# Kernel tuning notes

Hardware: AMD Instinct MI355X
Metric: run time of the kernel (lower is better)

The kernel has to match this reference:

```python
import jax, jax.numpy as jnp
import numpy as np

LAYERS, HIDDEN, FFN, HEADS = 2, 128, 256, 4
IMG_H, IMG_W = 32, 64
SEQ = IMG_H * IMG_W
HEAD = HIDDEN // HEADS          # 32, per-head qk dim
HEAD_V = 2 * HEAD               # double_v_dim=True
VDIM = HEADS * HEAD_V           # 256
B = 2
SCALE_BASE = 512.0
EPS = 1e-5


def _xpos_tables(seq, d):
    # XPOS: rotary angles + per-position exponential scale
    half = d // 2
    scale_vec = (jnp.arange(0, d, 2, dtype=jnp.float32) + 0.4 * d) / (1.4 * d)  # (d/2,)
    power = jnp.arange(seq, dtype=jnp.float32) / SCALE_BASE
    scale = scale_vec[None, :] ** power[:, None]                                 # (S, d/2)
    inv_freq = 1.0 / (10000.0 ** (jnp.arange(half, dtype=jnp.float32) / half))
    ang = jnp.arange(seq, dtype=jnp.float32)[:, None] * inv_freq[None, :]        # (S, d/2)
    return jnp.sin(ang), jnp.cos(ang), scale


def _apply_xpos(x, sin, cos, scale):
    # duplicate-interleave sin/cos*scale to width d, rotate-every-two
    s = jnp.repeat(sin * scale, 2, axis=-1)   # (S, d)
    c = jnp.repeat(cos * scale, 2, axis=-1)
    x1, x2 = x[..., ::2], x[..., 1::2]
    rot = jnp.stack([-x2, x1], axis=-1).reshape(x.shape)
    return x * c + rot * s


def _ln(x, g, b):
    mu = x.mean(-1, keepdims=True)
    var = ((x - mu) ** 2).mean(-1, keepdims=True)
    return (x - mu) * jax.lax.rsqrt(var + EPS) * g + b


def _gn(y, g, b):
    # GroupNorm(HEADS groups) over VDIM channels, applied per token
    bsz, s, v = y.shape
    yg = y.reshape(bsz, s, HEADS, HEAD_V)
    mu = yg.mean(-1, keepdims=True)
    var = ((yg - mu) ** 2).mean(-1, keepdims=True)
    yn = ((yg - mu) * jax.lax.rsqrt(var + EPS)).reshape(bsz, s, v)
    return yn * g + b


def _decay(seq):
    # D[h, n, m] = gamma_h^(n-m) for n >= m else 0
    gammas = 1.0 - jnp.exp(jnp.linspace(jnp.log(1.0 / 32.0), jnp.log(1.0 / 512.0), HEADS))
    n = jnp.arange(seq, dtype=jnp.float32)
    diff = n[:, None] - n[None, :]
    return (gammas[:, None, None] ** jnp.maximum(diff, 0.0)) * (diff >= 0.0)


def _forward(x, ln1_g, ln1_b, ln2_g, ln2_b, WQ, WK, WV, WG, WO, gn_g, gn_b, w1, b1, w2, b2):
    sin, cos, scale = _xpos_tables(SEQ, HEAD)
    D = _decay(SEQ)  # (H, S, S)
    for i in range(LAYERS):
        h = _ln(x, ln1_g[i], ln1_b[i])
        Q = _apply_xpos(jnp.einsum('bsd,hde->bhse', h, WQ[i]), sin, cos, scale)
        K = _apply_xpos(jnp.einsum('bsd,hde->bhse', h, WK[i]), sin, cos, 1.0 / scale)
        V = jnp.einsum('bsd,hdv->bhsv', h, WV[i])
        att = jnp.einsum('bhse,bhte->bhst', Q, K) * D[None]      # decay retention
        Y = jnp.einsum('bhst,bhtv->bhsv', att, V)
        Y = jnp.moveaxis(Y, 1, 2).reshape(x.shape[0], SEQ, VDIM)  # concat heads
        Y = _gn(Y, gn_g[i], gn_b[i])
        G = h @ WG[i]
        ret = (G * jax.nn.sigmoid(G) * Y) @ WO[i]                 # swish gate + out proj
        y = ret + x
        h2 = _ln(y, ln2_g[i], ln2_b[i])
        x = jax.nn.gelu(h2 @ w1[i] + b1[i], approximate=False) @ w2[i] + b2[i] + y
    return x.reshape(x.shape[0], IMG_H, IMG_W, x.shape[-1])


def setup_inputs() -> dict:
    key = jax.random.key(0)
    ks = jax.random.split(key, 8)
    def rn(k, shape, sc):
        return jax.random.normal(k, shape, dtype=jnp.float32) * sc
    s = 1.0 / np.sqrt(HIDDEN)
    return {
        'x': rn(ks[0], (B, SEQ, HIDDEN), 1.0),
        'ln1_g': jnp.ones((LAYERS, HIDDEN), jnp.float32),
        'ln1_b': jnp.zeros((LAYERS, HIDDEN), jnp.float32),
        'ln2_g': jnp.ones((LAYERS, HIDDEN), jnp.float32),
        'ln2_b': jnp.zeros((LAYERS, HIDDEN), jnp.float32),
        'WQ': rn(ks[1], (LAYERS, HEADS, HIDDEN, HEAD), s),
        'WK': rn(ks[2], (LAYERS, HEADS, HIDDEN, HEAD), s),
        'WV': rn(ks[3], (LAYERS, HEADS, HIDDEN, HEAD_V), s),
        'WG': rn(ks[4], (LAYERS, HIDDEN, VDIM), s),
        'WO': rn(ks[5], (LAYERS, VDIM, HIDDEN), 1.0 / np.sqrt(VDIM)),
        'gn_g': jnp.ones((LAYERS, VDIM), jnp.float32),
        'gn_b': jnp.zeros((LAYERS, VDIM), jnp.float32),
        'w1': rn(ks[6], (LAYERS, HIDDEN, FFN), s),
        'b1': jnp.zeros((LAYERS, FFN), jnp.float32),
        'w2': rn(ks[7], (LAYERS, FFN, HIDDEN), 1.0 / np.sqrt(FFN)),
        'b2': jnp.zeros((LAYERS, HIDDEN), jnp.float32),
    }


def reference(x, ln1_g, ln1_b, ln2_g, ln2_b, WQ, WK, WV, WG, WO, gn_g, gn_b, w1, b1, w2, b2):
    return _forward(x, ln1_g, ln1_b, ln2_g, ln2_b, WQ, WK, WV, WG, WO, gn_g, gn_b, w1, b1, w2, b2)
```

## Files before the change

### kernel.cpp

```cpp
#include <hip/hip_runtime.h>
#include <math.h>

#define NLAYERS 2
#define HID 128
#define FFND 256
#define NH 4
#define SEQL 2048
#define HD 32
#define HDV 64
#define VD 256
#define NBATCH 2
#define MROWS (NBATCH*SEQL)
#define NCAT 768
#define NCHUNK 32

__global__ __launch_bounds__(256) void setup_kernel(
    const float* __restrict__ WQ, const float* __restrict__ WK,
    const float* __restrict__ WV, const float* __restrict__ WG,
    float* __restrict__ Wcat, float* __restrict__ tabs)
{
  int bid = blockIdx.x;
  if (bid < 768) {
    int idx = bid * 256 + threadIdx.x;
    int l = idx / (HID * NCAT);
    int r = idx - l * (HID * NCAT);
    int k = r / NCAT;
    int n = r - k * NCAT;
    float v;
    if (n < 128)      { int h = n >> 5, e = n & 31;            v = WQ[(((l*NH+h)*HID)+k)*HD  + e]; }
    else if (n < 256) { int m = n-128; int h = m>>5, e = m&31; v = WK[(((l*NH+h)*HID)+k)*HD  + e]; }
    else if (n < 512) { int m = n-256; int h = m>>6, e = m&63; v = WV[(((l*NH+h)*HID)+k)*HDV + e]; }
    else              { v = WG[(l*HID + k)*VD + (n-512)]; }
    Wcat[idx] = v;
  } else {
    int idx = (bid - 768) * 256 + threadIdx.x;
    int s = idx >> 4, i = idx & 15;
    float inv_freq = powf(10000.f, -(float)i * (1.f/16.f));
    float ang = (float)s * inv_freq;
    float sv  = ((float)(2*i) + 0.4f*32.f) / (1.4f*32.f);
    float sc  = powf(sv, (float)s * (1.f/512.f));
    float sn = sinf(ang), cs = cosf(ang);
    tabs[idx]          = sn * sc;
    tabs[32768 + idx]  = cs * sc;
    tabs[65536 + idx]  = sn / sc;
    tabs[98304 + idx]  = cs / sc;
  }
}

template<int CN, bool XPOS, bool BIAS, bool GELU>
__global__ __launch_bounds__(256) void gemm_ln(
    const float* __restrict__ A, const float* __restrict__ Bw,
    const float* __restrict__ lng, const float* __restrict__ lnb,
    const float* __restrict__ bias, const float* __restrict__ tabs,
    float* __restrict__ C, int N)
{
  constexpr int TN = 16 * CN;
  constexpr int BK = (CN == 8) ? 32 : 64;
  __shared__ float As[128][68];
  __shared__ float Bs[BK][TN + 4];

  int tid = threadIdx.x;
  int tx = tid & 15, ty = tid >> 4;
  int rb = blockIdx.x * 64, nb = blockIdx.y * TN;

  {
    int row = tid >> 2, q = tid & 3;
    const float* ar = A + (size_t)(rb + row) * HID + 32 * q;
    float4 av[8];
    #pragma unroll
    for (int it = 0; it < 8; it++) av[it] = *(const float4*)(ar + 4*it);
    float s = 0.f;
    #pragma unroll
    for (int it = 0; it < 8; it++) s += av[it].x + av[it].y + av[it].z + av[it].w;
    s += __shfl_xor(s, 1); s += __shfl_xor(s, 2);
    float mu = s * (1.f/128.f);
    float qs = 0.f;
    #pragma unroll
    for (int it = 0; it < 8; it++) {
      float d;
      d = av[it].x - mu; qs += d*d;  d = av[it].y - mu; qs += d*d;
      d = av[it].z - mu; qs += d*d;  d = av[it].w - mu; qs += d*d;
    }
    qs += __shfl_xor(qs, 1); qs += __shfl_xor(qs, 2);
    float rs = rsqrtf(qs * (1.f/128.f) + 1e-5f);
    int rsw = row ^ (16 * q);
    #pragma unroll
    for (int it = 0; it < 8; it++) {
      int k0 = 32*q + 4*it;
      float4 g4 = *(const float4*)(lng + k0);
      float4 b4 = *(const float4*)(lnb + k0);
      As[k0+0][rsw] = (av[it].x-mu)*rs*g4.x + b4.x;
      As[k0+1][rsw] = (av[it].y-mu)*rs*g4.y + b4.y;
      As[k0+2][rsw] = (av[it].z-mu)*rs*g4.z + b4.z;
      As[k0+3][rsw] = (av[it].w-mu)*rs*g4.w + b4.w;
    }
  }

  float acc[4][CN];
  #pragma unroll
  for (int i=0;i<4;i++)
    #pragma unroll
    for (int j=0;j<CN;j++) acc[i][j] = 0.f;

  for (int ks = 0; ks < 128; ks += BK) {
    #pragma unroll
    for (int it = 0; it < 4; it++) {
      int idx = it*256 + tid;
      int kk = idx / (TN/4), nq = idx % (TN/4);
      *(float4*)(&Bs[kk][4*nq]) =
          *(const float4*)(Bw + (size_t)(ks+kk)*N + nb + 4*nq);
    }
    __syncthreads();
    #pragma unroll
    for (int kk = 0; kk < BK; kk++) {
      int k = ks + kk;
      float a[4];
      *(float4*)a = *(const float4*)&As[k][(4*ty) ^ (16*(k>>5))];
      float b[CN];
      #pragma unroll
      for (int j4 = 0; j4 < CN; j4 += 4)
        *(float4*)(b+j4) = *(const float4*)&Bs[kk][CN*tx + j4];
      #pragma unroll
      for (int i=0;i<4;i++)
        #pragma unroll
        for (int j=0;j<CN;j++)
          acc[i][j] = fmaf(a[i], b[j], acc[i][j]);
    }
    __syncthreads();
  }

  #pragma unroll
  for (int i=0;i<4;i++) {
    int row = rb + 4*ty + i;
    int cb = nb + CN*tx;
    float o[CN];
    #pragma unroll
    for (int j=0;j<CN;j++) {
      float v = acc[i][j];
      if (BIAS)  v += bias[cb + j];
      if (GELU)  v = 0.5f * v * (1.f + erff(v * 0.70710678118f));
      o[j] = v;
    }
    if (XPOS) {
      if (nb < 256) {
        bool isK = (nb >= 128);
        const float* sn_t = tabs + (isK ? 65536 : 0);
        const float* cs_t = tabs + (isK ? 98304 : 32768);
        int s = row & (SEQL - 1);
        #pragma unroll
        for (int p = 0; p < CN/2; p++) {
          int i0 = ((cb + 2*p) & 31) >> 1;
          float sn = sn_t[s*16 + i0], cs = cs_t[s*16 + i0];
          float x1 = o[2*p], x2 = o[2*p+1];
          o[2*p]   = x1*cs - x2*sn;
          o[2*p+1] = x2*cs + x1*sn;
        }
      }
    }
    #pragma unroll
    for (int j4 = 0; j4 < CN; j4 += 4)
      *(float4*)(C + (size_t)row*N + cb + j4) = *(float4*)(o + j4);
  }
}

template<bool BIAS>
__global__ __launch_bounds__(256) void gemm_nar(
    const float* __restrict__ A, const float* __restrict__ Bw,
    const float* __restrict__ bias, const float* __restrict__ Rsd,
    float* __restrict__ C, int N)
{
  __shared__ float As[64][68];
  __shared__ float Bs[64][36];
  int tid = threadIdx.x;
  int tx = tid & 15, ty = tid >> 4;
  int rb = blockIdx.x * 64, nb = blockIdx.y * 32;

  float acc[4][2];
  #pragma unroll
  for (int i=0;i<4;i++) { acc[i][0]=0.f; acc[i][1]=0.f; }

  for (int ks = 0; ks < 256; ks += 64) {
    #pragma unroll
    for (int it = 0; it < 4; it++) {
      int idx = it*256 + tid;
      int row = idx >> 4, kq = idx & 15;
      float4 a4 = *(const float4*)(A + (size_t)(rb+row)*256 + ks + 4*kq);
      int rsw = row ^ (4*(kq & 7));
      As[4*kq+0][rsw] = a4.x; As[4*kq+1][rsw] = a4.y;
      As[4*kq+2][rsw] = a4.z; As[4*kq+3][rsw] = a4.w;
    }
    #pragma unroll
    for (int it = 0; it < 2; it++) {
      int idx = it*256 + tid;
      int kk = idx >> 3, nq = idx & 7;
      *(float4*)(&Bs[kk][4*nq]) =
          *(const float4*)(Bw + (size_t)(ks+kk)*N + nb + 4*nq);
    }
    __syncthreads();
    #pragma unroll
    for (int kk = 0; kk < 64; kk++) {
      float a[4];
      *(float4*)a = *(const float4*)&As[kk][(4*ty) ^ (4*((kk>>2)&7))];
      float2 b2 = *(const float2*)&Bs[kk][2*tx];
      #pragma unroll
      for (int i=0;i<4;i++) {
        acc[i][0] = fmaf(a[i], b2.x, acc[i][0]);
        acc[i][1] = fmaf(a[i], b2.y, acc[i][1]);
      }
    }
    __syncthreads();
  }

  #pragma unroll
  for (int i=0;i<4;i++) {
    int row = rb + 4*ty + i;
    int cb = nb + 2*tx;
    float o[2];
    #pragma unroll
    for (int j=0;j<2;j++) {
      float v = acc[i][j];
      if (BIAS) v += bias[cb + j];
      v += Rsd[(size_t)row*N + cb + j];
      o[j] = v;
    }
    *(float2*)(C + (size_t)row*N + cb) = *(float2*)o;
  }
}

__global__ __launch_bounds__(512) void ret_kv_kernel(
    const float* __restrict__ QKVG, float* __restrict__ Asum)
{
  int bh = blockIdx.x >> 5;
  int c  = blockIdx.x & 31;
  int b = bh >> 2, h = bh & 3;
  float t0 = logf(1.f/32.f) + (float)h * (logf(1.f/512.f) - logf(1.f/32.f)) * (1.f/3.f);
  float gamma = 1.f - expf(t0);
  float lg = logf(gamma);

  __shared__ float Ks[64][36];
  __shared__ float Vs[64][68];
  __shared__ float wt[64];

  int tid = threadIdx.x;
  int c0 = c * 64;
  const float* base = QKVG + (size_t)(b * SEQL) * NCAT;

  {
    int row = tid >> 3, eq = tid & 7;
    *(float4*)&Ks[row][4*eq] =
        *(const float4*)(base + (size_t)(c0+row)*NCAT + 128 + h*32 + 4*eq);
  }
  #pragma unroll
  for (int it = 0; it < 2; it++) {
    int idx = it*512 + tid;
    int row = idx >> 4, vq = idx & 15;
    *(float4*)&Vs[row][4*vq] =
        *(const float4*)(base + (size_t)(c0+row)*NCAT + 256 + h*64 + 4*vq);
  }
  if (tid < 64) wt[tid] = __expf(lg * (float)(64 - tid));
  __syncthreads();

  int e = tid >> 4, v4 = (tid & 15) * 4;
  float a0[4] = {0,0,0,0};
  #pragma unroll 8
  for (int t = 0; t < 64; t++) {
    float kw = Ks[t][e] * wt[t];
    float4 v0 = *(const float4*)&Vs[t][v4];
    a0[0] = fmaf(kw, v0.x, a0[0]); a0[1] = fmaf(kw, v0.y, a0[1]);
    a0[2] = fmaf(kw, v0.z, a0[2]); a0[3] = fmaf(kw, v0.w, a0[3]);
  }
  *(float4*)(Asum + ((size_t)(bh*NCHUNK + c))*2048 + e*64 + v4) = *(float4*)a0;
}

__global__ __launch_bounds__(512) void ret_out_kernel(
    const float* __restrict__ QKVG, const float* __restrict__ Asum,
    const float* __restrict__ gn_g, const float* __restrict__ gn_b,
    float* __restrict__ Gated)
{
  int bh = blockIdx.x >> 5;
  int c  = blockIdx.x & 31;
  int b = bh >> 2, h = bh & 3;
  float t0 = logf(1.f/32.f) + (float)h * (logf(1.f/512.f) - logf(1.f/32.f)) * (1.f/3.f);
  float gamma = 1.f - expf(t0);
  float lg = logf(gamma);
  float g64 = __expf(lg * 64.f);

  __shared__ float Qs[64][36];
  __shared__ float Ks[64][36];
  __shared__ float Vs[64][68];
  __shared__ float Ss[64][68];
  __shared__ float Sc[32][68];

  int tid = threadIdx.x;
  int tx2 = tid & 31, ty2 = tid >> 5;
  int c0 = c * 64;
  const float* base = QKVG + (size_t)(b * SEQL) * NCAT;

  {
    int row = tid >> 3, eq = tid & 7;
    *(float4*)&Qs[row][4*eq] =
        *(const float4*)(base + (size_t)(c0+row)*NCAT + h*32 + 4*eq);
    int esw = (4*eq) ^ (4*((row >> 2) & 7));
    *(float4*)&Ks[row][esw] =
        *(const float4*)(base + (size_t)(c0+row)*NCAT + 128 + h*32 + 4*eq);
  }
  #pragma unroll
  for (int it = 0; it < 2; it++) {
    int idx = it*512 + tid;
    int row = idx >> 4, vq = idx & 15;
    *(float4*)&Vs[row][4*vq] =
        *(const float4*)(base + (size_t)(c0+row)*NCAT + 256 + h*64 + 4*vq);
  }

  {
    int e = tid >> 4, v4 = (tid & 15) * 4;
    float s0[4] = {0,0,0,0};
    float w = 1.f;
    const float* ab = Asum + ((size_t)bh*NCHUNK)*2048 + e*64 + v4;
    for (int cp = c-1; cp >= 0; --cp) {
      const float* ap = ab + (size_t)cp*2048;
      float4 x0 = *(const float4*)ap;
      s0[0] = fmaf(w, x0.x, s0[0]); s0[1] = fmaf(w, x0.y, s0[1]);
      s0[2] = fmaf(w, x0.z, s0[2]); s0[3] = fmaf(w, x0.w, s0[3]);
      w *= g64;
    }
    *(float4*)&Sc[e][v4] = *(float4*)s0;
  }
  __syncthreads();

  float sacc[4][2];
  #pragma unroll
  for (int i=0;i<4;i++) { sacc[i][0]=0.f; sacc[i][1]=0.f; }
  #pragma unroll
  for (int e = 0; e < 32; e += 4) {
    float qv[4][4], kv[2][4];
    #pragma unroll
    for (int i=0;i<4;i++)
      *(float4*)qv[i] = *(const float4*)&Qs[4*ty2+i][e];
    #pragma unroll
    for (int j=0;j<2;j++) {
      int kr = 2*tx2 + j;
      *(float4*)kv[j] = *(const float4*)&Ks[kr][e ^ (4*((kr>>2)&7))];
    }
    #pragma unroll
    for (int i=0;i<4;i++)
      #pragma unroll
      for (int j=0;j<2;j++)
        sacc[i][j] = fmaf(qv[i][0], kv[j][0],
                     fmaf(qv[i][1], kv[j][1],
                     fmaf(qv[i][2], kv[j][2],
                     fmaf(qv[i][3], kv[j][3], sacc[i][j]))));
  }
  #pragma unroll
  for (int i=0;i<4;i++) {
    int sl = 4*ty2 + i;
    float o2[2];
    #pragma unroll
    for (int j=0;j<2;j++) {
      int dr = sl - (2*tx2 + j);
      float w = (dr >= 0) ? __expf(lg * (float)dr) : 0.f;
      o2[j] = sacc[i][j] * w;
    }
    *(float2*)&Ss[sl][2*tx2] = *(float2*)o2;
  }

  float acc[4][2];
  #pragma unroll
  for (int i=0;i<4;i++) { acc[i][0]=0.f; acc[i][1]=0.f; }
  #pragma unroll
  for (int e = 0; e < 32; e += 4) {
    float qv[4][4], sv[4][2];
    #pragma unroll
    for (int i=0;i<4;i++)
      *(float4*)qv[i] = *(const float4*)&Qs[4*ty2+i][e];
    #pragma unroll
    for (int m=0;m<4;m++)
      *(float2*)sv[m] = *(const float2*)&Sc[e+m][2*tx2];
    #pragma unroll
    for (int i=0;i<4;i++)
      #pragma unroll
      for (int j=0;j<2;j++)
        acc[i][j] = fmaf(qv[i][0], sv[0][j],
                    fmaf(qv[i][1], sv[1][j],
                    fmaf(qv[i][2], sv[2][j],
                    fmaf(qv[i][3], sv[3][j], acc[i][j]))));
  }
  #pragma unroll
  for (int i=0;i<4;i++) {
    float gr = __expf(lg * (float)(4*ty2 + i));
    acc[i][0] *= gr; acc[i][1] *= gr;
  }
  __syncthreads();

  #pragma unroll
  for (int t = 0; t < 64; t += 4) {
    float sv[4][4], vv[4][2];
    #pragma unroll
    for (int i=0;i<4;i++)
      *(float4*)sv[i] = *(const float4*)&Ss[4*ty2+i][t];
    #pragma unroll
    for (int m=0;m<4;m++)
      *(float2*)vv[m] = *(const float2*)&Vs[t+m][2*tx2];
    #pragma unroll
    for (int i=0;i<4;i++)
      #pragma unroll
      for (int j=0;j<2;j++)
        acc[i][j] = fmaf(sv[i][0], vv[0][j],
                    fmaf(sv[i][1], vv[1][j],
                    fmaf(sv[i][2], vv[2][j],
                    fmaf(sv[i][3], vv[3][j], acc[i][j]))));
  }

  #pragma unroll
  for (int i=0;i<4;i++) {
    float s1 = acc[i][0] + acc[i][1];
    #pragma unroll
    for (int o = 16; o; o >>= 1) s1 += __shfl_xor(s1, o);
    float mu = s1 * (1.f/64.f);
    float q = 0.f;
    #pragma unroll
    for (int j=0;j<2;j++) { float d = acc[i][j] - mu; q += d*d; }
    #pragma unroll
    for (int o = 16; o; o >>= 1) q += __shfl_xor(q, o);
    float rs = rsqrtf(q * (1.f/64.f) + 1e-5f);
    int row = b*SEQL + c0 + 4*ty2 + i;
    float2 g2 = *(const float2*)(QKVG + (size_t)row*NCAT + 512 + h*64 + 2*tx2);
    float gv[2] = {g2.x, g2.y};
    float o2[2];
    #pragma unroll
    for (int j=0;j<2;j++) {
      int col = h*64 + 2*tx2 + j;
      float yn = (acc[i][j] - mu) * rs * gn_g[col] + gn_b[col];
      float g = gv[j];
      float sig = 1.f / (1.f + __expf(-g));
      o2[j] = g * sig * yn;
    }
    *(float2*)(Gated + (size_t)row*VD + h*64 + 2*tx2) = *(float2*)o2;
  }
}

extern "C" void kernel_launch(void* const* d_in, const int* in_sizes, int n_in,
                              void* d_out, int out_size, void* d_ws, size_t ws_size,
                              hipStream_t stream)
{
  (void)in_sizes; (void)n_in; (void)out_size; (void)ws_size;
  const float* x_in  = (const float*)d_in[0];
  const float* ln1_g = (const float*)d_in[1];
  const float* ln1_b = (const float*)d_in[2];
  const float* ln2_g = (const float*)d_in[3];
  const float* ln2_b = (const float*)d_in[4];
  const float* WQ    = (const float*)d_in[5];
  const float* WK    = (const float*)d_in[6];
  const float* WV    = (const float*)d_in[7];
  const float* WG    = (const float*)d_in[8];
  const float* WO    = (const float*)d_in[9];
  const float* gn_g  = (const float*)d_in[10];
  const float* gn_b  = (const float*)d_in[11];
  const float* w1    = (const float*)d_in[12];
  const float* b1    = (const float*)d_in[13];
  const float* w2    = (const float*)d_in[14];
  const float* b2    = (const float*)d_in[15];
  float* out = (float*)d_out;
  float* ws  = (float*)d_ws;

  float* Wcat = ws;
  float* tabs = Wcat + 196608;
  float* QKVG = tabs + 131072;
  float* Asum = QKVG + 3145728;
  float* Gt   = Asum + 524288;
  float* Yres = Gt   + 1048576;
  float* Mid  = Yres + 524288;

  setup_kernel<<<896, 256, 0, stream>>>(WQ, WK, WV, WG, Wcat, tabs);

  for (int l = 0; l < NLAYERS; l++) {
    const float* xl = (l == 0) ? x_in : out;
    gemm_ln<8,true,false,false><<<dim3(MROWS/64, NCAT/128), 256, 0, stream>>>(
        xl, Wcat + l*HID*NCAT, ln1_g + l*HID, ln1_b + l*HID,
        nullptr, tabs, QKVG, NCAT);
    ret_kv_kernel<<<256, 512, 0, stream>>>(QKVG, Asum);
    ret_out_kernel<<<256, 512, 0, stream>>>(QKVG, Asum, gn_g + l*VD, gn_b + l*VD, Gt);
    gemm_nar<false><<<dim3(MROWS/64, HID/32), 256, 0, stream>>>(
        Gt, WO + l*VD*HID, nullptr, xl, Yres, HID);
    gemm_ln<4,false,true,true><<<dim3(MROWS/64, FFND/64), 256, 0, stream>>>(
        Yres, w1 + l*HID*FFND, ln2_g + l*HID, ln2_b + l*HID,
        b1 + l*FFND, nullptr, Mid, FFND);
    gemm_nar<true><<<dim3(MROWS/64, HID/32), 256, 0, stream>>>(
        Mid, w2 + l*FFND*HID, b2 + l*HID, Yres, out, HID);
  }
}
```

Baseline: 236.5 us.

## Split LayerNorm into own kernel and retile projection GEMMs with register prefetch

Moves LayerNorm out of the GEMM prologue into a standalone wave-per-row kernel writing a normalized buffer. The QKVG GEMM now reads WQ/WK/WV/WG directly with computed column offsets instead of a pre-concatenated weight copy. It uses 64-thread blocks with 8x8 register tiles and register-prefetched weight tiles. The FFN1 and output GEMMs are retiled to larger per-thread outputs with fewer threads. This adds two LN launches and an extra activation round trip in exchange for higher arithmetic intensity per thread and dropping the weight-concatenation setup.

```diff
diff --git a/kernel.cpp b/kernel.cpp
--- a/kernel.cpp
+++ b/kernel.cpp
@@ -14,199 +14,280 @@
 #define NCAT 768
 #define NCHUNK 32
 
-__global__ __launch_bounds__(256) void setup_kernel(
+__global__ __launch_bounds__(256) void tabs_kernel(float* __restrict__ tabs)
+{
+  int idx = blockIdx.x * 256 + threadIdx.x;
+  int s = idx >> 4, i = idx & 15;
+  float inv_freq = powf(10000.f, -(float)i * (1.f/16.f));
+  float ang = (float)s * inv_freq;
+  float sv  = ((float)(2*i) + 0.4f*32.f) / (1.4f*32.f);
+  float sc  = powf(sv, (float)s * (1.f/512.f));
+  float sn = sinf(ang), cs = cosf(ang);
+  tabs[idx]          = sn * sc;
+  tabs[32768 + idx]  = cs * sc;
+  tabs[65536 + idx]  = sn / sc;
+  tabs[98304 + idx]  = cs / sc;
+}
+
+__global__ __launch_bounds__(256) void ln_rows_kernel(
+    const float* __restrict__ X, const float* __restrict__ g,
+    const float* __restrict__ b, float* __restrict__ O)
+{
+  int wid = threadIdx.x >> 6, lane = threadIdx.x & 63;
+  int row = blockIdx.x * 4 + wid;
+  const float* x = X + (size_t)row * HID;
+  float v0 = x[lane], v1 = x[lane + 64];
+  float s = v0 + v1;
+  #pragma unroll
+  for (int o = 32; o; o >>= 1) s += __shfl_xor(s, o);
+  float mu = s * (1.f/128.f);
+  float d0 = v0 - mu, d1 = v1 - mu;
+  float q = d0*d0 + d1*d1;
+  #pragma unroll
+  for (int o = 32; o; o >>= 1) q += __shfl_xor(q, o);
+  float rs = rsqrtf(q * (1.f/128.f) + 1e-5f);
+  O[(size_t)row*HID + lane]      = d0 * rs * g[lane]      + b[lane];
+  O[(size_t)row*HID + lane + 64] = d1 * rs * g[lane + 64] + b[lane + 64];
+}
+
+__global__ __launch_bounds__(64) void gemm_qkvg(
+    const float* __restrict__ H,
     const float* __restrict__ WQ, const float* __restrict__ WK,
     const float* __restrict__ WV, const float* __restrict__ WG,
-    float* __restrict__ Wcat, float* __restrict__ tabs)
-{
-  int bid = blockIdx.x;
-  if (bid < 768) {
-    int idx = bid * 256 + threadIdx.x;
-    int l = idx / (HID * NCAT);
-    int r = idx - l * (HID * NCAT);
-    int k = r / NCAT;
-    int n = r - k * NCAT;
-    float v;
-    if (n < 128)      { int h = n >> 5, e = n & 31;            v = WQ[(((l*NH+h)*HID)+k)*HD  + e]; }
-    else if (n < 256) { int m = n-128; int h = m>>5, e = m&31; v = WK[(((l*NH+h)*HID)+k)*HD  + e]; }
-    else if (n < 512) { int m = n-256; int h = m>>6, e = m&63; v = WV[(((l*NH+h)*HID)+k)*HDV + e]; }
-    else              { v = WG[(l*HID + k)*VD + (n-512)]; }
-    Wcat[idx] = v;
-  } else {
-    int idx = (bid - 768) * 256 + threadIdx.x;
-    int s = idx >> 4, i = idx & 15;
-    float inv_freq = powf(10000.f, -(float)i * (1.f/16.f));
-    float ang = (float)s * inv_freq;
-    float sv  = ((float)(2*i) + 0.4f*32.f) / (1.4f*32.f);
-    float sc  = powf(sv, (float)s * (1.f/512.f));
-    float sn = sinf(ang), cs = cosf(ang);
-    tabs[idx]          = sn * sc;
-    tabs[32768 + idx]  = cs * sc;
-    tabs[65536 + idx]  = sn / sc;
-    tabs[98304 + idx]  = cs / sc;
-  }
-}
-
-template<int CN, bool XPOS, bool BIAS, bool GELU>
-__global__ __launch_bounds__(256) void gemm_ln(
-    const float* __restrict__ A, const float* __restrict__ Bw,
-    const float* __restrict__ lng, const float* __restrict__ lnb,
-    const float* __restrict__ bias, const float* __restrict__ tabs,
-    float* __restrict__ C, int N)
-{
-  constexpr int TN = 16 * CN;
-  constexpr int BK = (CN == 8) ? 32 : 64;
+    const float* __restrict__ tabs, float* __restrict__ C, int l)
+{
   __shared__ float As[128][68];
-  __shared__ float Bs[BK][TN + 4];
-
+  __shared__ float Bs[32][68];
   int tid = threadIdx.x;
-  int tx = tid & 15, ty = tid >> 4;
-  int rb = blockIdx.x * 64, nb = blockIdx.y * TN;
-
-  {
-    int row = tid >> 2, q = tid & 3;
-    const float* ar = A + (size_t)(rb + row) * HID + 32 * q;
-    float4 av[8];
-    #pragma unroll
-    for (int it = 0; it < 8; it++) av[it] = *(const float4*)(ar + 4*it);
-    float s = 0.f;
-    #pragma unroll
-    for (int it = 0; it < 8; it++) s += av[it].x + av[it].y + av[it].z + av[it].w;
-    s += __shfl_xor(s, 1); s += __shfl_xor(s, 2);
-    float mu = s * (1.f/128.f);
-    float qs = 0.f;
+  int tx = tid & 7, ty = tid >> 3;
+  int rb = blockIdx.x * 64, nb = blockIdx.y * 64;
+
+  const float* wbase; int kstr;
+  if (nb < 128)      { wbase = WQ + (size_t)l*NH*HID*HD;  kstr = HD;  }
+  else if (nb < 256) { wbase = WK + (size_t)l*NH*HID*HD;  kstr = HD;  }
+  else if (nb < 512) { wbase = WV + (size_t)l*NH*HID*HDV; kstr = HDV; }
+  else               { wbase = WG + (size_t)l*HID*VD;     kstr = VD;  }
+  int coffs[8];
+  #pragma unroll
+  for (int it = 0; it < 8; it++) {
+    int nq = (it*64 + tid) & 15;
+    int n = nb + 4*nq;
+    int co;
+    if (nb < 128)      co = (n>>5)*(HID*HD) + (n&31);
+    else if (nb < 256) { int m = n-128; co = (m>>5)*(HID*HD)  + (m&31); }
+    else if (nb < 512) { int m = n-256; co = (m>>6)*(HID*HDV) + (m&63); }
+    else               co = n - 512;
+    coffs[it] = co;
+  }
+
+  #pragma unroll
+  for (int it = 0; it < 32; it++) {
+    int idx = it*64 + tid;
+    int row = idx >> 5, f4q = idx & 31;
+    float4 a4 = *(const float4*)(H + (size_t)(rb+row)*HID + 4*f4q);
+    int rs = row ^ (8*(f4q & 7));
+    As[4*f4q+0][rs] = a4.x; As[4*f4q+1][rs] = a4.y;
+    As[4*f4q+2][rs] = a4.z; As[4*f4q+3][rs] = a4.w;
+  }
+
+  float4 pre[8];
+  #pragma unroll
+  for (int it = 0; it < 8; it++) {
+    int kk = ((it*64 + tid) >> 4);
+    pre[it] = *(const float4*)(wbase + (size_t)kk*kstr + coffs[it]);
+  }
+
+  float acc[8][8];
+  #pragma unroll
+  for (int i=0;i<8;i++)
+    #pragma unroll
+    for (int j=0;j<8;j++) acc[i][j] = 0.f;
+
+  for (int ks = 0; ks < 128; ks += 32) {
+    __syncthreads();
     #pragma unroll
     for (int it = 0; it < 8; it++) {
-      float d;
-      d = av[it].x - mu; qs += d*d;  d = av[it].y - mu; qs += d*d;
-      d = av[it].z - mu; qs += d*d;  d = av[it].w - mu; qs += d*d;
-    }
-    qs += __shfl_xor(qs, 1); qs += __shfl_xor(qs, 2);
-    float rs = rsqrtf(qs * (1.f/128.f) + 1e-5f);
-    int rsw = row ^ (16 * q);
+      int idx = it*64 + tid;
+      int kk = idx >> 4, nq = idx & 15;
+      *(float4*)&Bs[kk][4*nq] = pre[it];
+    }
+    __syncthreads();
+    if (ks + 32 < 128) {
+      #pragma unroll
+      for (int it = 0; it < 8; it++) {
+        int kk = ((it*64 + tid) >> 4);
+        pre[it] = *(const float4*)(wbase + (size_t)(ks+32+kk)*kstr + coffs[it]);
+      }
+    }
+    #pragma unroll
+    for (int kk = 0; kk < 32; kk++) {
+      int k = ks + kk;
+      int sw = (8*ty) ^ (8*((k>>2)&7));
+      float a[8], b[8];
+      *(float4*)(a)   = *(const float4*)&As[k][sw];
+      *(float4*)(a+4) = *(const float4*)&As[k][sw + 4];
+      *(float4*)(b)   = *(const float4*)&Bs[kk][8*tx];
+      *(float4*)(b+4) = *(const float4*)&Bs[kk][8*tx + 4];
+      #pragma unroll
+      for (int i=0;i<8;i++)
+        #pragma unroll
+        for (int j=0;j<8;j++)
+          acc[i][j] = fmaf(a[i], b[j], acc[i][j]);
+    }
+  }
+
+  #pragma unroll
+  for (int i=0;i<8;i++) {
+    int row = rb + 8*ty + i;
+    int cb = nb + 8*tx;
+    float o[8];
+    #pragma unroll
+    for (int j=0;j<8;j++) o[j] = acc[i][j];
+    if (nb < 256) {
+      bool isK = (nb >= 128);
+      const float* sn_t = tabs + (isK ? 65536 : 0);
+      const float* cs_t = tabs + (isK ? 98304 : 32768);
+      int s = row & (SEQL - 1);
+      #pragma unroll
+      for (int p = 0; p < 4; p++) {
+        int i0 = ((cb + 2*p) & 31) >> 1;
+        float sn = sn_t[s*16 + i0], cs = cs_t[s*16 + i0];
+        float x1 = o[2*p], x2 = o[2*p+1];
+        o[2*p]   = x1*cs - x2*sn;
+        o[2*p+1] = x2*cs + x1*sn;
+      }
+    }
+    *(float4*)(C + (size_t)row*NCAT + cb)     = *(float4*)(o);
+    *(float4*)(C + (size_t)row*NCAT + cb + 4) = *(float4*)(o + 4);
+  }
+}
+
+__global__ __launch_bounds__(64) void gemm_ffn1(
+    const float* __restrict__ H, const float* __restrict__ Bw,
+    const float* __restrict__ bias, float* __restrict__ C)
+{
+  __shared__ float As[128][36];
+  __shared__ float Bs[32][68];
+  int tid = threadIdx.x;
+  int tx = tid & 7, ty = tid >> 3;
+  int rb = blockIdx.x * 32, nb = blockIdx.y * 64;
+
+  #pragma unroll
+  for (int it = 0; it < 16; it++) {
+    int idx = it*64 + tid;
+    int row = idx >> 5, f4q = idx & 31;
+    float4 a4 = *(const float4*)(H + (size_t)(rb+row)*HID + 4*f4q);
+    int rs = row ^ (4*(f4q & 7));
+    As[4*f4q+0][rs] = a4.x; As[4*f4q+1][rs] = a4.y;
+    As[4*f4q+2][rs] = a4.z; As[4*f4q+3][rs] = a4.w;
+  }
+
+  float4 pre[8];
+  #pragma unroll
+  for (int it = 0; it < 8; it++) {
+    int idx = it*64 + tid;
+    int kk = idx >> 4, nq = idx & 15;
+    pre[it] = *(const float4*)(Bw + (size_t)kk*FFND + nb + 4*nq);
+  }
+
+  float acc[4][8];
+  #pragma unroll
+  for (int i=0;i<4;i++)
+    #pragma unroll
+    for (int j=0;j<8;j++) acc[i][j] = 0.f;
+
+  for (int ks = 0; ks < 128; ks += 32) {
+    __syncthreads();
     #pragma unroll
     for (int it = 0; it < 8; it++) {
-      int k0 = 32*q + 4*it;
-      float4 g4 = *(const float4*)(lng + k0);
-      float4 b4 = *(const float4*)(lnb + k0);
-      As[k0+0][rsw] = (av[it].x-mu)*rs*g4.x + b4.x;
-      As[k0+1][rsw] = (av[it].y-mu)*rs*g4.y + b4.y;
-      As[k0+2][rsw] = (av[it].z-mu)*rs*g4.z + b4.z;
-      As[k0+3][rsw] = (av[it].w-mu)*rs*g4.w + b4.w;
-    }
-  }
-
-  float acc[4][CN];
-  #pragma unroll
-  for (int i=0;i<4;i++)
-    #pragma unroll
-    for (int j=0;j<CN;j++) acc[i][j] = 0.f;
-
-  for (int ks = 0; ks < 128; ks += BK) {
-    #pragma unroll
-    for (int it = 0; it < 4; it++) {
-      int idx = it*256 + tid;
-      int kk = idx / (TN/4), nq = idx % (TN/4);
-      *(float4*)(&Bs[kk][4*nq]) =
-          *(const float4*)(Bw + (size_t)(ks+kk)*N + nb + 4*nq);
+      int idx = it*64 + tid;
+      int kk = idx >> 4, nq = idx & 15;
+      *(float4*)&Bs[kk][4*nq] = pre[it];
     }
     __syncthreads();
-    #pragma unroll
-    for (int kk = 0; kk < BK; kk++) {
+    if (ks + 32 < 128) {
+      #pragma unroll
+      for (int it = 0; it < 8; it++) {
+        int idx = it*64 + tid;
+        int kk = idx >> 4, nq = idx & 15;
+        pre[it] = *(const float4*)(Bw + (size_t)(ks+32+kk)*FFND + nb + 4*nq);
+      }
+    }
+    #pragma unroll
+    for (int kk = 0; kk < 32; kk++) {
       int k = ks + kk;
-      float a[4];
-      *(float4*)a = *(const float4*)&As[k][(4*ty) ^ (16*(k>>5))];
-      float b[CN];
-      #pragma unroll
-      for (int j4 = 0; j4 < CN; j4 += 4)
-        *(float4*)(b+j4) = *(const float4*)&Bs[kk][CN*tx + j4];
+      float a[4], b[8];
+      *(float4*)a     = *(const float4*)&As[k][(4*ty) ^ (4*((k>>2)&7))];
+      *(float4*)(b)   = *(const float4*)&Bs[kk][8*tx];
+      *(float4*)(b+4) = *(const float4*)&Bs[kk][8*tx + 4];
       #pragma unroll
       for (int i=0;i<4;i++)
         #pragma unroll
-        for (int j=0;j<CN;j++)
+        for (int j=0;j<8;j++)
           acc[i][j] = fmaf(a[i], b[j], acc[i][j]);
     }
-    __syncthreads();
   }
 
   #pragma unroll
   for (int i=0;i<4;i++) {
     int row = rb + 4*ty + i;
-    int cb = nb + CN*tx;
-    float o[CN];
-    #pragma unroll
-    for (int j=0;j<CN;j++) {
-      float v = acc[i][j];
-      if (BIAS)  v += bias[cb + j];
-      if (GELU)  v = 0.5f * v * (1.f + erff(v * 0.70710678118f));
-      o[j] = v;
-    }
-    if (XPOS) {
-      if (nb < 256) {
-        bool isK = (nb >= 128);
-        const float* sn_t = tabs + (isK ? 65536 : 0);
-        const float* cs_t = tabs + (isK ? 98304 : 32768);
-        int s = row & (SEQL - 1);
-        #pragma unroll
-        for (int p = 0; p < CN/2; p++) {
-          int i0 = ((cb + 2*p) & 31) >> 1;
-          float sn = sn_t[s*16 + i0], cs = cs_t[s*16 + i0];
-          float x1 = o[2*p], x2 = o[2*p+1];
-          o[2*p]   = x1*cs - x2*sn;
-          o[2*p+1] = x2*cs + x1*sn;
-        }
-      }
-    }
-    #pragma unroll
-    for (int j4 = 0; j4 < CN; j4 += 4)
-      *(float4*)(C + (size_t)row*N + cb + j4) = *(float4*)(o + j4);
+    int cb = nb + 8*tx;
+    float o[8];
+    #pragma unroll
+    for (int j=0;j<8;j++) {
+      float v = acc[i][j] + bias[cb + j];
+      o[j] = 0.5f * v * (1.f + erff(v * 0.70710678118f));
+    }
+    *(float4*)(C + (size_t)row*FFND + cb)     = *(float4*)(o);
+    *(float4*)(C + (size_t)row*FFND + cb + 4) = *(float4*)(o + 4);
   }
 }
 
 template<bool BIAS>
-__global__ __launch_bounds__(256) void gemm_nar(
+__global__ __launch_bounds__(128) void gemm_nar(
     const float* __restrict__ A, const float* __restrict__ Bw,
     const float* __restrict__ bias, const float* __restrict__ Rsd,
-    float* __restrict__ C, int N)
+    float* __restrict__ C)
 {
   __shared__ float As[64][68];
   __shared__ float Bs[64][36];
   int tid = threadIdx.x;
-  int tx = tid & 15, ty = tid >> 4;
+  int tx = tid & 7, ty = tid >> 3;
   int rb = blockIdx.x * 64, nb = blockIdx.y * 32;
 
-  float acc[4][2];
-  #pragma unroll
-  for (int i=0;i<4;i++) { acc[i][0]=0.f; acc[i][1]=0.f; }
+  float acc[4][4];
+  #pragma unroll
+  for (int i=0;i<4;i++)
+    #pragma unroll
+    for (int j=0;j<4;j++) acc[i][j] = 0.f;
 
   for (int ks = 0; ks < 256; ks += 64) {
     #pragma unroll
-    for (int it = 0; it < 4; it++) {
-      int idx = it*256 + tid;
+    for (int it = 0; it < 8; it++) {
+      int idx = it*128 + tid;
       int row = idx >> 4, kq = idx & 15;
       float4 a4 = *(const float4*)(A + (size_t)(rb+row)*256 + ks + 4*kq);
-      int rsw = row ^ (4*(kq & 7));
-      As[4*kq+0][rsw] = a4.x; As[4*kq+1][rsw] = a4.y;
-      As[4*kq+2][rsw] = a4.z; As[4*kq+3][rsw] = a4.w;
-    }
-    #pragma unroll
-    for (int it = 0; it < 2; it++) {
-      int idx = it*256 + tid;
+      int rs = row ^ (4*(kq & 7));
+      As[4*kq+0][rs] = a4.x; As[4*kq+1][rs] = a4.y;
+      As[4*kq+2][rs] = a4.z; As[4*kq+3][rs] = a4.w;
+    }
+    #pragma unroll
+    for (int it = 0; it < 4; it++) {
+      int idx = it*128 + tid;
       int kk = idx >> 3, nq = idx & 7;
-      *(float4*)(&Bs[kk][4*nq]) =
-          *(const float4*)(Bw + (size_t)(ks+kk)*N + nb + 4*nq);
+      *(float4*)&Bs[kk][4*nq] = *(const float4*)(Bw + (size_t)(ks+kk)*HID + nb + 4*nq);
     }
     __syncthreads();
     #pragma unroll
     for (int kk = 0; kk < 64; kk++) {
-      float a[4];
+      float a[4], b[4];
       *(float4*)a = *(const float4*)&As[kk][(4*ty) ^ (4*((kk>>2)&7))];
-      float2 b2 = *(const float2*)&Bs[kk][2*tx];
-      #pragma unroll
-      for (int i=0;i<4;i++) {
-        acc[i][0] = fmaf(a[i], b2.x, acc[i][0]);
-        acc[i][1] = fmaf(a[i], b2.y, acc[i][1]);
-      }
+      *(float4*)b = *(const float4*)&Bs[kk][4*tx];
+      #pragma unroll
+      for (int i=0;i<4;i++)
+        #pragma unroll
+        for (int j=0;j<4;j++)
+          acc[i][j] = fmaf(a[i], b[j], acc[i][j]);
     }
     __syncthreads();
   }
@@ -214,16 +295,16 @@
   #pragma unroll
   for (int i=0;i<4;i++) {
     int row = rb + 4*ty + i;
-    int cb = nb + 2*tx;
-    float o[2];
-    #pragma unroll
-    for (int j=0;j<2;j++) {
+    int cb = nb + 4*tx;
+    float o[4];
+    #pragma unroll
+    for (int j=0;j<4;j++) {
       float v = acc[i][j];
       if (BIAS) v += bias[cb + j];
-      v += Rsd[(size_t)row*N + cb + j];
+      v += Rsd[(size_t)row*HID + cb + j];
       o[j] = v;
     }
-    *(float2*)(C + (size_t)row*N + cb) = *(float2*)o;
+    *(float4*)(C + (size_t)row*HID + cb) = *(float4*)o;
   }
 }
 
@@ -463,29 +544,29 @@
   float* out = (float*)d_out;
   float* ws  = (float*)d_ws;
 
-  float* Wcat = ws;
-  float* tabs = Wcat + 196608;
-  float* QKVG = tabs + 131072;
+  float* tabs = ws;
+  float* Hbuf = tabs + 131072;
+  float* QKVG = Hbuf + 524288;
   float* Asum = QKVG + 3145728;
   float* Gt   = Asum + 524288;
   float* Yres = Gt   + 1048576;
   float* Mid  = Yres + 524288;
 
-  setup_kernel<<<896, 256, 0, stream>>>(WQ, WK, WV, WG, Wcat, tabs);
+  tabs_kernel<<<128, 256, 0, stream>>>(tabs);
 
   for (int l = 0; l < NLAYERS; l++) {
     const float* xl = (l == 0) ? x_in : out;
-    gemm_ln<8,true,false,false><<<dim3(MROWS/64, NCAT/128), 256, 0, stream>>>(
-        xl, Wcat + l*HID*NCAT, ln1_g + l*HID, ln1_b + l*HID,
-        nullptr, tabs, QKVG, NCAT);
+    ln_rows_kernel<<<MROWS/4, 256, 0, stream>>>(xl, ln1_g + l*HID, ln1_b + l*HID, Hbuf);
+    gemm_qkvg<<<dim3(MROWS/64, NCAT/64), 64, 0, stream>>>(
+        Hbuf, WQ, WK, WV, WG, tabs, QKVG, l);
     ret_kv_kernel<<<256, 512, 0, stream>>>(QKVG, Asum);
     ret_out_kernel<<<256, 512, 0, stream>>>(QKVG, Asum, gn_g + l*VD, gn_b + l*VD, Gt);
-    gemm_nar<false><<<dim3(MROWS/64, HID/32), 256, 0, stream>>>(
-        Gt, WO + l*VD*HID, nullptr, xl, Yres, HID);
-    gemm_ln<4,false,true,true><<<dim3(MROWS/64, FFND/64), 256, 0, stream>>>(
-        Yres, w1 + l*HID*FFND, ln2_g + l*HID, ln2_b + l*HID,
-        b1 + l*FFND, nullptr, Mid, FFND);
-    gemm_nar<true><<<dim3(MROWS/64, HID/32), 256, 0, stream>>>(
-        Mid, w2 + l*FFND*HID, b2 + l*HID, Yres, out, HID);
-  }
-}
+    gemm_nar<false><<<dim3(MROWS/64, HID/32), 128, 0, stream>>>(
+        Gt, WO + l*VD*HID, nullptr, xl, Yres);
+    ln_rows_kernel<<<MROWS/4, 256, 0, stream>>>(Yres, ln2_g + l*HID, ln2_b + l*HID, Hbuf);
+    gemm_ffn1<<<dim3(MROWS/32, FFND/64), 64, 0, stream>>>(
+        Hbuf, w1 + l*HID*FFND, b1 + l*FFND, Mid);
+    gemm_nar<true><<<dim3(MROWS/64, HID/32), 128, 0, stream>>>(
+        Mid, w2 + l*FFND*HID, b2 + l*HID, Yres, out);
+  }
+}
```

Result: slower. 269.3 us (+13.9%).
